# Kernel tuning notes

Measured on AMD Instinct MI355X. Metric: run time of the kernel, lower is better.

The kernel has to match this reference:

```python
import jax, jax.numpy as jnp
import numpy as np

N, D, H, Y = 2048, 768, 12, 64


def setup_inputs() -> dict:
    key = jax.random.key(0)
    kg, kq, kk = jax.random.split(key, 3)
    g = jax.random.normal(kg, (N, D), dtype=jnp.float32)
    Wq = jax.random.normal(kq, (H, Y, D), dtype=jnp.float32)
    Wk = jax.random.normal(kk, (H, Y, D), dtype=jnp.float32)
    return {"g": g, "Wq": Wq, "Wk": Wk}


def reference(g, Wq, Wk):
    # g: [N, D]; Wq, Wk: [H, Y, D]
    beta = 1.0 / jnp.sqrt(jnp.asarray(Y, dtype=g.dtype))
    K = jnp.einsum('kd,hzd->khz', g, Wk)          # [N, H, Y]
    Q = jnp.einsum('qd,hzd->qhz', g, Wq)          # [N, H, Y]
    scores = beta * jnp.einsum('qhz,khz->hqk', Q, K)  # [H, N, N]
    A = jax.nn.logsumexp(scores, axis=-1)         # [H, N]
    return (-1.0 / beta) * A.sum()
```

## Files before the change

kernel.cpp:

```cpp
#include <hip/hip_runtime.h>
#include <hip/hip_bf16.h>

#define NN 2048
#define DD 768
#define HH 12
#define HW 1536
#define G_ELEMS (NN*DD)
#define W1_ELEMS (HH*64*DD)
#define SPLITS 4
#define KPW (NN/SPLITS)

typedef __attribute__((ext_vector_type(8))) short bf16x8;
typedef __attribute__((ext_vector_type(4))) float f32x4;

__device__ __forceinline__ float exp2g(float x) { return __builtin_amdgcn_exp2f(x); }
__device__ __forceinline__ float log2g(float x) { return __builtin_amdgcn_logf(x); }

#define QSCALE 0.18033688011112042f
__global__ __launch_bounds__(256) void convert_kernel(
    const float* __restrict__ g, const float* __restrict__ Wq,
    const float* __restrict__ Wk, __hip_bfloat16* __restrict__ gB,
    __hip_bfloat16* __restrict__ wB) {
  int base = (blockIdx.x * 256 + threadIdx.x) * 4;
  float4 v;
  __hip_bfloat16* dst;
  if (base < G_ELEMS) {
    v = *reinterpret_cast<const float4*>(g + base);
    dst = gB + base;
  } else if (base < G_ELEMS + W1_ELEMS) {
    int o = base - G_ELEMS;
    v = *reinterpret_cast<const float4*>(Wq + o);
    v.x *= QSCALE; v.y *= QSCALE; v.z *= QSCALE; v.w *= QSCALE;
    dst = wB + o;
  } else {
    int o = base - (G_ELEMS + W1_ELEMS);
    v = *reinterpret_cast<const float4*>(Wk + o);
    dst = wB + W1_ELEMS + o;
  }
  __hip_bfloat16 h0 = __float2bfloat16(v.x), h1 = __float2bfloat16(v.y);
  __hip_bfloat16 h2 = __float2bfloat16(v.z), h3 = __float2bfloat16(v.w);
  ushort4 u;
  u.x = *reinterpret_cast<unsigned short*>(&h0);
  u.y = *reinterpret_cast<unsigned short*>(&h1);
  u.z = *reinterpret_cast<unsigned short*>(&h2);
  u.w = *reinterpret_cast<unsigned short*>(&h3);
  *reinterpret_cast<ushort4*>(dst) = u;
}

#define LDP 72
__global__ __launch_bounds__(256) void proj_kernel(
    const __hip_bfloat16* __restrict__ gB, const __hip_bfloat16* __restrict__ wB,
    __hip_bfloat16* __restrict__ QK) {
  __shared__ __align__(16) __hip_bfloat16 As[64 * LDP];
  __shared__ __align__(16) __hip_bfloat16 Bs[64 * LDP];
  const int t = threadIdx.x;
  const int wave = t >> 6, lane = t & 63;
  const int lr = lane & 15, lg = lane >> 4;
  const int wm = wave & 1, wn = wave >> 1;
  const int bm = blockIdx.x, bn = blockIdx.y;

  f32x4 acc[2][2] = {};

  for (int kt = 0; kt < DD; kt += 64) {
    __syncthreads();
#pragma unroll
    for (int i = 0; i < 2; ++i) {
      int c = t + i * 256;
      int row = c >> 3, seg = (c & 7) * 8;
      uint4 va = *reinterpret_cast<const uint4*>(gB + (bm * 64 + row) * DD + kt + seg);
      *reinterpret_cast<uint4*>(&As[row * LDP + seg]) = va;
      uint4 vb = *reinterpret_cast<const uint4*>(wB + (bn * 64 + row) * DD + kt + seg);
      *reinterpret_cast<uint4*>(&Bs[row * LDP + seg]) = vb;
    }
    __syncthreads();
#pragma unroll
    for (int ks = 0; ks < 2; ++ks) {
      bf16x8 a[2], b[2];
#pragma unroll
      for (int mt = 0; mt < 2; ++mt)
        a[mt] = *reinterpret_cast<const bf16x8*>(&As[(wm * 32 + mt * 16 + lr) * LDP + ks * 32 + lg * 8]);
#pragma unroll
      for (int nt = 0; nt < 2; ++nt)
        b[nt] = *reinterpret_cast<const bf16x8*>(&Bs[(wn * 32 + nt * 16 + lr) * LDP + ks * 32 + lg * 8]);
#pragma unroll
      for (int mt = 0; mt < 2; ++mt)
#pragma unroll
        for (int nt = 0; nt < 2; ++nt)
          acc[mt][nt] = __builtin_amdgcn_mfma_f32_16x16x32_bf16(a[mt], b[nt], acc[mt][nt], 0, 0, 0);
    }
  }
#pragma unroll
  for (int mt = 0; mt < 2; ++mt) {
    int row = bm * 64 + wm * 32 + mt * 16 + lg * 4;
#pragma unroll
    for (int nt = 0; nt < 2; ++nt) {
      int col = bn * 64 + wn * 32 + nt * 16 + lr;
#pragma unroll
      for (int r = 0; r < 4; ++r)
        QK[(row + r) * HW + col] = __float2bfloat16(acc[mt][nt][r]);
    }
  }
}

#define LDA 72
__global__ __launch_bounds__(256) void attn_kernel(
    const __hip_bfloat16* __restrict__ QK, float2* __restrict__ part) {
  __shared__ __align__(16) __hip_bfloat16 Qs[64 * LDA];
  __shared__ __align__(16) __hip_bfloat16 Ks[64 * LDA];
  const int t = threadIdx.x;
  const int wave = t >> 6, lane = t & 63;
  const int lr = lane & 15, lg = lane >> 4;
  const int q0 = blockIdx.x * 64, h = blockIdx.y, sp = blockIdx.z;
  const int k0 = sp * KPW;

#pragma unroll
  for (int i = 0; i < 2; ++i) {
    int c = t + i * 256;
    int row = c >> 3, seg = (c & 7) * 8;
    uint4 v = *reinterpret_cast<const uint4*>(QK + (q0 + row) * HW + h * 64 + seg);
    *reinterpret_cast<uint4*>(&Qs[row * LDA + seg]) = v;
  }
  __syncthreads();
  bf16x8 aq[2];
#pragma unroll
  for (int z = 0; z < 2; ++z)
    aq[z] = *reinterpret_cast<const bf16x8*>(&Qs[(wave * 16 + lr) * LDA + z * 32 + lg * 8]);

  float m[4], l[4];
#pragma unroll
  for (int r = 0; r < 4; ++r) { m[r] = -3.0e38f; l[r] = 0.0f; }

  for (int kc = k0; kc < k0 + KPW; kc += 64) {
    __syncthreads();
#pragma unroll
    for (int i = 0; i < 2; ++i) {
      int c = t + i * 256;
      int row = c >> 3, seg = (c & 7) * 8;
      uint4 v = *reinterpret_cast<const uint4*>(QK + (kc + row) * HW + DD + h * 64 + seg);
      *reinterpret_cast<uint4*>(&Ks[row * LDA + seg]) = v;
    }
    __syncthreads();
    f32x4 s[4] = {};
#pragma unroll
    for (int nt = 0; nt < 4; ++nt)
#pragma unroll
      for (int z = 0; z < 2; ++z) {
        bf16x8 b = *reinterpret_cast<const bf16x8*>(&Ks[(nt * 16 + lr) * LDA + z * 32 + lg * 8]);
        s[nt] = __builtin_amdgcn_mfma_f32_16x16x32_bf16(aq[z], b, s[nt], 0, 0, 0);
      }
#pragma unroll
    for (int r = 0; r < 4; ++r) {
      float v0 = s[0][r], v1 = s[1][r], v2 = s[2][r], v3 = s[3][r];
      float cm = fmaxf(fmaxf(v0, v1), fmaxf(v2, v3));
      float mn = fmaxf(m[r], cm);
      float p = exp2g(v0 - mn) + exp2g(v1 - mn) +
                exp2g(v2 - mn) + exp2g(v3 - mn);
      l[r] = l[r] * exp2g(m[r] - mn) + p;
      m[r] = mn;
    }
  }
#pragma unroll
  for (int msk = 1; msk <= 8; msk <<= 1) {
#pragma unroll
    for (int r = 0; r < 4; ++r) {
      float mo = __shfl_xor(m[r], msk);
      float lo = __shfl_xor(l[r], msk);
      float mn = fmaxf(m[r], mo);
      l[r] = l[r] * exp2g(m[r] - mn) + lo * exp2g(mo - mn);
      m[r] = mn;
    }
  }
  if (lr == 0) {
#pragma unroll
    for (int r = 0; r < 4; ++r) {
      int q = q0 + wave * 16 + lg * 4 + r;
      part[(sp * HH + h) * NN + q] = make_float2(m[r], l[r]);
    }
  }
}

__global__ __launch_bounds__(256) void reduce_kernel(
    const float2* __restrict__ part, float* __restrict__ out) {
  const int t = threadIdx.x;
  const int row = blockIdx.x * 256 + t;
  float2 p0 = part[row];
  float2 p1 = part[24576 + row];
  float2 p2 = part[49152 + row];
  float2 p3 = part[73728 + row];
  float m = fmaxf(fmaxf(p0.x, p1.x), fmaxf(p2.x, p3.x));
  float l = p0.y * exp2g(p0.x - m) + p1.y * exp2g(p1.x - m) +
            p2.y * exp2g(p2.x - m) + p3.y * exp2g(p3.x - m);
  float lse = m + log2g(l);
#pragma unroll
  for (int msk = 1; msk <= 32; msk <<= 1)
    lse += __shfl_xor(lse, msk);
  __shared__ float wsum[4];
  if ((t & 63) == 0) wsum[t >> 6] = lse;
  __syncthreads();
  if (t == 0)
    atomicAdd(out, -5.545177444479562f * (wsum[0] + wsum[1] + wsum[2] + wsum[3]));
}

extern "C" void kernel_launch(void* const* d_in, const int* in_sizes, int n_in,
                              void* d_out, int out_size, void* d_ws, size_t ws_size,
                              hipStream_t stream) {
  const float* g  = (const float*)d_in[0];
  const float* Wq = (const float*)d_in[1];
  const float* Wk = (const float*)d_in[2];
  float* out = (float*)d_out;

  __hip_bfloat16* gB = (__hip_bfloat16*)d_ws;
  __hip_bfloat16* wB = gB + G_ELEMS;
  __hip_bfloat16* QK = wB + 2 * W1_ELEMS;
  float2* part = (float2*)gB;

  (void)hipMemsetAsync(d_out, 0, sizeof(float), stream);
  convert_kernel<<<2688, 256, 0, stream>>>(g, Wq, Wk, gB, wB);
  proj_kernel<<<dim3(32, 24), 256, 0, stream>>>(gB, wB, QK);
  attn_kernel<<<dim3(32, HH, SPLITS), 256, 0, stream>>>(QK, part);
  reduce_kernel<<<96, 256, 0, stream>>>(part, out);
}
```

Baseline: 106.8 us.

## Load attention tiles directly into registers, double Q rows per wave, single-block reduce

```diff
diff --git a/kernel.cpp b/kernel.cpp
--- a/kernel.cpp
+++ b/kernel.cpp
@@ -102,103 +102,111 @@
   }
 }
 
-#define LDA 72
 __global__ __launch_bounds__(256) void attn_kernel(
     const __hip_bfloat16* __restrict__ QK, float2* __restrict__ part) {
-  __shared__ __align__(16) __hip_bfloat16 Qs[64 * LDA];
-  __shared__ __align__(16) __hip_bfloat16 Ks[64 * LDA];
   const int t = threadIdx.x;
   const int wave = t >> 6, lane = t & 63;
   const int lr = lane & 15, lg = lane >> 4;
-  const int q0 = blockIdx.x * 64, h = blockIdx.y, sp = blockIdx.z;
+  const int q0 = blockIdx.x * 128, h = blockIdx.y, sp = blockIdx.z;
   const int k0 = sp * KPW;
-
-#pragma unroll
-  for (int i = 0; i < 2; ++i) {
-    int c = t + i * 256;
-    int row = c >> 3, seg = (c & 7) * 8;
-    uint4 v = *reinterpret_cast<const uint4*>(QK + (q0 + row) * HW + h * 64 + seg);
-    *reinterpret_cast<uint4*>(&Qs[row * LDA + seg]) = v;
-  }
-  __syncthreads();
-  bf16x8 aq[2];
-#pragma unroll
-  for (int z = 0; z < 2; ++z)
-    aq[z] = *reinterpret_cast<const bf16x8*>(&Qs[(wave * 16 + lr) * LDA + z * 32 + lg * 8]);
-
-  float m[4], l[4];
-#pragma unroll
-  for (int r = 0; r < 4; ++r) { m[r] = -3.0e38f; l[r] = 0.0f; }
+  const int colQ = h * 64 + lg * 8;
+  const int colK = DD + h * 64 + lg * 8;
+
+  bf16x8 aq[2][2];
+#pragma unroll
+  for (int mt = 0; mt < 2; ++mt)
+#pragma unroll
+    for (int z = 0; z < 2; ++z)
+      aq[mt][z] = *reinterpret_cast<const bf16x8*>(
+          QK + (q0 + wave * 32 + mt * 16 + lr) * HW + colQ + z * 32);
+
+  float m[2][4], l[2][4];
+#pragma unroll
+  for (int mt = 0; mt < 2; ++mt)
+#pragma unroll
+    for (int r = 0; r < 4; ++r) { m[mt][r] = -3.0e38f; l[mt][r] = 0.0f; }
 
   for (int kc = k0; kc < k0 + KPW; kc += 64) {
-    __syncthreads();
-#pragma unroll
-    for (int i = 0; i < 2; ++i) {
-      int c = t + i * 256;
-      int row = c >> 3, seg = (c & 7) * 8;
-      uint4 v = *reinterpret_cast<const uint4*>(QK + (kc + row) * HW + DD + h * 64 + seg);
-      *reinterpret_cast<uint4*>(&Ks[row * LDA + seg]) = v;
-    }
-    __syncthreads();
-    f32x4 s[4] = {};
+    bf16x8 b[4][2];
 #pragma unroll
     for (int nt = 0; nt < 4; ++nt)
 #pragma unroll
-      for (int z = 0; z < 2; ++z) {
-        bf16x8 b = *reinterpret_cast<const bf16x8*>(&Ks[(nt * 16 + lr) * LDA + z * 32 + lg * 8]);
-        s[nt] = __builtin_amdgcn_mfma_f32_16x16x32_bf16(aq[z], b, s[nt], 0, 0, 0);
+      for (int z = 0; z < 2; ++z)
+        b[nt][z] = *reinterpret_cast<const bf16x8*>(
+            QK + (kc + nt * 16 + lr) * HW + colK + z * 32);
+
+    f32x4 s[2][4] = {};
+#pragma unroll
+    for (int mt = 0; mt < 2; ++mt)
+#pragma unroll
+      for (int nt = 0; nt < 4; ++nt)
+#pragma unroll
+        for (int z = 0; z < 2; ++z)
+          s[mt][nt] = __builtin_amdgcn_mfma_f32_16x16x32_bf16(aq[mt][z], b[nt][z], s[mt][nt], 0, 0, 0);
+
+#pragma unroll
+    for (int mt = 0; mt < 2; ++mt)
+#pragma unroll
+      for (int r = 0; r < 4; ++r) {
+        float v0 = s[mt][0][r], v1 = s[mt][1][r], v2 = s[mt][2][r], v3 = s[mt][3][r];
+        float cm = fmaxf(fmaxf(v0, v1), fmaxf(v2, v3));
+        float mn = fmaxf(m[mt][r], cm);
+        float p = exp2g(v0 - mn) + exp2g(v1 - mn) +
+                  exp2g(v2 - mn) + exp2g(v3 - mn);
+        l[mt][r] = l[mt][r] * exp2g(m[mt][r] - mn) + p;
+        m[mt][r] = mn;
       }
-#pragma unroll
-    for (int r = 0; r < 4; ++r) {
-      float v0 = s[0][r], v1 = s[1][r], v2 = s[2][r], v3 = s[3][r];
-      float cm = fmaxf(fmaxf(v0, v1), fmaxf(v2, v3));
-      float mn = fmaxf(m[r], cm);
-      float p = exp2g(v0 - mn) + exp2g(v1 - mn) +
-                exp2g(v2 - mn) + exp2g(v3 - mn);
-      l[r] = l[r] * exp2g(m[r] - mn) + p;
-      m[r] = mn;
-    }
   }
 #pragma unroll
   for (int msk = 1; msk <= 8; msk <<= 1) {
 #pragma unroll
-    for (int r = 0; r < 4; ++r) {
-      float mo = __shfl_xor(m[r], msk);
-      float lo = __shfl_xor(l[r], msk);
-      float mn = fmaxf(m[r], mo);
-      l[r] = l[r] * exp2g(m[r] - mn) + lo * exp2g(mo - mn);
-      m[r] = mn;
-    }
+    for (int mt = 0; mt < 2; ++mt)
+#pragma unroll
+      for (int r = 0; r < 4; ++r) {
+        float mo = __shfl_xor(m[mt][r], msk);
+        float lo = __shfl_xor(l[mt][r], msk);
+        float mn = fmaxf(m[mt][r], mo);
+        l[mt][r] = l[mt][r] * exp2g(m[mt][r] - mn) + lo * exp2g(mo - mn);
+        m[mt][r] = mn;
+      }
   }
   if (lr == 0) {
 #pragma unroll
-    for (int r = 0; r < 4; ++r) {
-      int q = q0 + wave * 16 + lg * 4 + r;
-      part[(sp * HH + h) * NN + q] = make_float2(m[r], l[r]);
-    }
-  }
-}
-
-__global__ __launch_bounds__(256) void reduce_kernel(
+    for (int mt = 0; mt < 2; ++mt)
+#pragma unroll
+      for (int r = 0; r < 4; ++r) {
+        int q = q0 + wave * 32 + mt * 16 + lg * 4 + r;
+        part[(sp * HH + h) * NN + q] = make_float2(m[mt][r], l[mt][r]);
+      }
+  }
+}
+
+__global__ __launch_bounds__(1024) void reduce_kernel(
     const float2* __restrict__ part, float* __restrict__ out) {
   const int t = threadIdx.x;
-  const int row = blockIdx.x * 256 + t;
-  float2 p0 = part[row];
-  float2 p1 = part[24576 + row];
-  float2 p2 = part[49152 + row];
-  float2 p3 = part[73728 + row];
-  float m = fmaxf(fmaxf(p0.x, p1.x), fmaxf(p2.x, p3.x));
-  float l = p0.y * exp2g(p0.x - m) + p1.y * exp2g(p1.x - m) +
-            p2.y * exp2g(p2.x - m) + p3.y * exp2g(p3.x - m);
-  float lse = m + log2g(l);
+  float acc = 0.0f;
+  for (int row = t; row < HH * NN; row += 1024) {
+    float2 p0 = part[row];
+    float2 p1 = part[24576 + row];
+    float2 p2 = part[49152 + row];
+    float2 p3 = part[73728 + row];
+    float m = fmaxf(fmaxf(p0.x, p1.x), fmaxf(p2.x, p3.x));
+    float l = p0.y * exp2g(p0.x - m) + p1.y * exp2g(p1.x - m) +
+              p2.y * exp2g(p2.x - m) + p3.y * exp2g(p3.x - m);
+    acc += m + log2g(l);
+  }
 #pragma unroll
   for (int msk = 1; msk <= 32; msk <<= 1)
-    lse += __shfl_xor(lse, msk);
-  __shared__ float wsum[4];
-  if ((t & 63) == 0) wsum[t >> 6] = lse;
+    acc += __shfl_xor(acc, msk);
+  __shared__ float wsum[16];
+  if ((t & 63) == 0) wsum[t >> 6] = acc;
   __syncthreads();
-  if (t == 0)
-    atomicAdd(out, -5.545177444479562f * (wsum[0] + wsum[1] + wsum[2] + wsum[3]));
+  if (t == 0) {
+    float s = 0.0f;
+#pragma unroll
+    for (int i = 0; i < 16; ++i) s += wsum[i];
+    out[0] = -5.545177444479562f * s;
+  }
 }
 
 extern "C" void kernel_launch(void* const* d_in, const int* in_sizes, int n_in,
@@ -214,9 +222,8 @@
   __hip_bfloat16* QK = wB + 2 * W1_ELEMS;
   float2* part = (float2*)gB;
 
-  (void)hipMemsetAsync(d_out, 0, sizeof(float), stream);
   convert_kernel<<<2688, 256, 0, stream>>>(g, Wq, Wk, gB, wB);
   proj_kernel<<<dim3(32, 24), 256, 0, stream>>>(gB, wB, QK);
-  attn_kernel<<<dim3(32, HH, SPLITS), 256, 0, stream>>>(QK, part);
-  reduce_kernel<<<96, 256, 0, stream>>>(part, out);
-}
+  attn_kernel<<<dim3(16, HH, SPLITS), 256, 0, stream>>>(QK, part);
+  reduce_kernel<<<1, 1024, 0, stream>>>(part, out);
+}
```

Result: slower. 120.6 us (+12.9%).
